# Kernel tuning notes

Measured on AMD Instinct MI355X. Metric: run time of the kernel, lower is better.

The kernel has to match this reference:

```python
import jax, jax.numpy as jnp
import numpy as np

B, T = 32, 64
INPUT_DIM, EMB, HA, HB, NUM_CLASS = 4894, 128, 128, 128, 1
D_IN = EMB + 1  # use_time=True appends scalar time feature


def gru_cell(x, h, Wih, Whh, bih, bhh):
    # torch nn.GRU cell semantics, gate order (r, z, n)
    gi = x @ Wih.T + bih
    gh = h @ Whh.T + bhh
    ir, iz, i_n = jnp.split(gi, 3, axis=-1)
    hr, hz, hn = jnp.split(gh, 3, axis=-1)
    r = jax.nn.sigmoid(ir + hr)
    z = jax.nn.sigmoid(iz + hz)
    n = jnp.tanh(i_n + r * hn)
    return (1.0 - z) * n + z * h


def setup_inputs():
    key = jax.random.key(0)
    ks = jax.random.split(key, 14)
    f32 = jnp.float32
    s = lambda k, sh, sc: (jax.random.normal(k, sh) * sc).astype(f32)
    return {
        "x": jax.random.uniform(ks[0], (B, T, INPUT_DIM), dtype=f32),
        "t": jax.random.uniform(ks[1], (B, T), dtype=f32),
        "lengths": jax.random.randint(ks[2], (B,), 1, T + 1),
        "W_emb": s(ks[3], (EMB, INPUT_DIM), 0.02),
        "Wih_a": s(ks[4], (3 * HA, D_IN), 0.05),
        "Whh_a": s(ks[5], (3 * HA, HA), 0.05),
        "bih_a": jnp.zeros((3 * HA,), f32),
        "bhh_a": jnp.zeros((3 * HA,), f32),
        "Wih_b": s(ks[6], (3 * HB, D_IN), 0.05),
        "Whh_b": s(ks[7], (3 * HB, HB), 0.05),
        "bih_b": jnp.zeros((3 * HB,), f32),
        "bhh_b": jnp.zeros((3 * HB,), f32),
        "w_alpha": s(ks[8], (1, HA), 0.1),
        "b_alpha": jnp.zeros((1,), f32),
        "W_beta": s(ks[9], (EMB, HB), 0.1),
        "b_beta": jnp.zeros((EMB,), f32),
        "W_out": s(ks[10], (NUM_CLASS, EMB), 0.1),
        "b_out": jnp.zeros((NUM_CLASS,), f32),
    }


def reference(x, t, lengths, W_emb, Wih_a, Whh_a, bih_a, bhh_a,
              Wih_b, Whh_b, bih_b, bhh_b, w_alpha, b_alpha,
              W_beta, b_beta, W_out, b_out):
    # embedding (dropout is identity in inference)
    emb = x @ W_emb.T                                   # [B,T,E]
    temb = jnp.concatenate([emb, t[..., None]], axis=-1)  # [B,T,E+1]

    # reversed-prefix tensor: R[b,i,k] = temb[b, i-k] for k<=i else 0
    i_idx = jnp.arange(T)[:, None]
    k_idx = jnp.arange(T)[None, :]
    src = i_idx - k_idx                                  # [T,T]
    valid = (src >= 0)
    src_c = jnp.clip(src, 0)
    vmask = valid[None, :, :, None].astype(emb.dtype)
    R = jnp.take(temb, src_c, axis=1) * vmask            # [B,T,T,D_IN]
    E_rev = jnp.take(emb, src_c, axis=1) * vmask         # [B,T,T,E]

    # run alpha/beta GRUs along the prefix axis k (causal, so zero padding
    # at k>i never affects the k<=i outputs that we keep)
    R_k = jnp.moveaxis(R, 2, 0)                          # [Tk,B,T,D_IN]
    h0a = jnp.zeros((B, T, HA), emb.dtype)
    h0b = jnp.zeros((B, T, HB), emb.dtype)

    def step(carry, xk):
        ha, hb = carry
        ha = gru_cell(xk, ha, Wih_a, Whh_a, bih_a, bhh_a)
        hb = gru_cell(xk, hb, Wih_b, Whh_b, bih_b, bhh_b)
        return (ha, hb), (ha, hb)

    _, (Ha, Hb) = jax.lax.scan(step, (h0a, h0b), R_k)
    Ha = jnp.moveaxis(Ha, 0, 2)                          # [B,T,Tk,HA]
    Hb = jnp.moveaxis(Hb, 0, 2)                          # [B,T,Tk,HB]

    # attention over the i+1 prefix positions
    scores = (Ha @ w_alpha.T + b_alpha)[..., 0]          # [B,T,Tk]
    scores = jnp.where(valid[None], scores, jnp.float32(-1e9))
    alpha = jax.nn.softmax(scores, axis=-1)
    beta = jnp.tanh(Hb @ W_beta.T + b_beta)              # [B,T,Tk,E]

    c = jnp.einsum('btk,btke,btke->bte', alpha, beta, E_rev)
    row_valid = (jnp.arange(T)[None, :] < lengths[:, None]).astype(c.dtype)
    c = c * row_valid[..., None]                         # zero where i >= lengths[b]

    logits = c @ W_out.T + b_out                         # [B,T,1]
    return logits[..., 0]
```

## Files before the change

kernel.cpp:

```cpp
#include <hip/hip_runtime.h>
#include <hip/hip_bf16.h>

#define DEVI __device__ __forceinline__

typedef __attribute__((ext_vector_type(8))) short short8;
typedef __attribute__((ext_vector_type(8))) unsigned short ushort8;
typedef __attribute__((ext_vector_type(4))) unsigned short ushort4v;
typedef __attribute__((ext_vector_type(2))) unsigned int u32x2;
typedef __attribute__((ext_vector_type(4))) float f32x4;

static constexpr int TT = 64, KIN = 4894, KINP = 4896, E = 128;
static constexpr float L2E = 1.4426950408889634f;

DEVI unsigned short f2bf(float f) {
    union { float f; unsigned u; } v; v.f = f;
    unsigned r = v.u + 0x7fffu + ((v.u >> 16) & 1u);
    return (unsigned short)(r >> 16);
}
DEVI float sigm2(float x) { return __builtin_amdgcn_rcpf(1.f + __builtin_amdgcn_exp2f(-x)); }
DEVI float tanh2(float x) { return 1.f - 2.f * __builtin_amdgcn_rcpf(__builtin_amdgcn_exp2f(x + x) + 1.f); }

DEVI void gload16(const float* g, float* l) {
    __builtin_amdgcn_global_load_lds(
        (const __attribute__((address_space(1))) void*)g,
        (__attribute__((address_space(3))) void*)l, 16, 0, 0);
}

DEVI short8 cvt8(const float* __restrict__ p, float s) {
    float2 v0 = *(const float2*)p, v1 = *(const float2*)(p + 2);
    float2 v2 = *(const float2*)(p + 4), v3 = *(const float2*)(p + 6);
    short8 r;
    r[0] = (short)f2bf(v0.x * s); r[1] = (short)f2bf(v0.y * s);
    r[2] = (short)f2bf(v1.x * s); r[3] = (short)f2bf(v1.y * s);
    r[4] = (short)f2bf(v2.x * s); r[5] = (short)f2bf(v2.y * s);
    r[6] = (short)f2bf(v3.x * s); r[7] = (short)f2bf(v3.y * s);
    return r;
}

__global__ void prep_kernel(const float* __restrict__ Wemb,
                            const float* __restrict__ Wih_a, const float* __restrict__ Wih_b,
                            const float* __restrict__ Whh_a, const float* __restrict__ Whh_b,
                            const float* __restrict__ Wbeta,
                            unsigned short* __restrict__ wembbf, unsigned short* __restrict__ wihbf,
                            unsigned short* __restrict__ whhbf, unsigned short* __restrict__ wbetabf) {
    int job = blockIdx.x * blockDim.x + threadIdx.x;
    const int JWE = 128 * 612, JWIH = 768 * 16, JWHH = 768 * 16, JWB = 128 * 16;
    if (job < JWE) {
        int row = job / 612, c8 = (job % 612) * 8;
        ushort8 v;
        #pragma unroll
        for (int jj = 0; jj < 8; ++jj) { int c = c8 + jj; v[jj] = (c < KIN) ? f2bf(Wemb[(long)row * KIN + c]) : (unsigned short)0; }
        *(ushort8*)(wembbf + (long)row * KINP + c8) = v;
        return;
    }
    job -= JWE;
    if (job < JWIH) {
        int g = job / 16, c8 = (job % 16) * 8;
        const float* src = (g < 384) ? (Wih_a + (long)g * 129) : (Wih_b + (long)(g - 384) * 129);
        ushort8 v;
        #pragma unroll
        for (int jj = 0; jj < 8; ++jj) v[jj] = f2bf(src[c8 + jj] * L2E);
        *(ushort8*)(wihbf + (long)g * 128 + c8) = v;
        return;
    }
    job -= JWIH;
    if (job < JWHH) {
        int g = job / 16, c8 = (job % 16) * 8;
        const float* src = (g < 384) ? (Whh_a + (long)g * 128) : (Whh_b + (long)(g - 384) * 128);
        ushort8 v;
        #pragma unroll
        for (int jj = 0; jj < 8; ++jj) v[jj] = f2bf(src[c8 + jj] * L2E);
        *(ushort8*)(whhbf + (long)g * 128 + c8) = v;
        return;
    }
    job -= JWHH;
    if (job < JWB) {
        int e = job / 16, c8 = (job % 16) * 8;
        ushort8 v;
        #pragma unroll
        for (int jj = 0; jj < 8; ++jj) v[jj] = f2bf(Wbeta[(long)e * 128 + c8 + jj] * L2E);
        *(ushort8*)(wbetabf + (long)e * 128 + c8) = v;
    }
}

__global__ __launch_bounds__(256) void emb_gemm(const float* __restrict__ x,
                                                const unsigned short* __restrict__ wembbf,
                                                float* __restrict__ pout) {
    const int ks = blockIdx.x & 3, m0 = (blockIdx.x >> 2) * 16;
    const int w = threadIdx.x >> 6, l = threadIdx.x & 63, lr = l & 15, lo = l >> 4;
    const int n0 = (2 * w) * 16 + lr, n1 = (2 * w + 1) * 16 + lr;
    const float* xrow = x + (long)(m0 + lr) * KIN;
    const int k0 = ks * 1216;
    f32x4 acc0 = {0, 0, 0, 0}, acc1 = {0, 0, 0, 0};
    #pragma unroll 2
    for (int kt = 0; kt < 38; ++kt) {
        int k = k0 + kt * 32 + lo * 8;
        short8 a = cvt8(xrow + k, 1.f);
        short8 b0 = *(const short8*)(wembbf + (long)n0 * KINP + k);
        short8 b1 = *(const short8*)(wembbf + (long)n1 * KINP + k);
        acc0 = __builtin_amdgcn_mfma_f32_16x16x32_bf16(a, b0, acc0, 0, 0, 0);
        acc1 = __builtin_amdgcn_mfma_f32_16x16x32_bf16(a, b1, acc1, 0, 0, 0);
    }
    if (ks == 3) {
        int k = 4864 + lo * 8;
        short8 a;
        #pragma unroll
        for (int jj = 0; jj < 8; ++jj) { int c = k + jj; a[jj] = (c < KIN) ? (short)f2bf(xrow[c]) : (short)0; }
        short8 b0 = *(const short8*)(wembbf + (long)n0 * KINP + k);
        short8 b1 = *(const short8*)(wembbf + (long)n1 * KINP + k);
        acc0 = __builtin_amdgcn_mfma_f32_16x16x32_bf16(a, b0, acc0, 0, 0, 0);
        acc1 = __builtin_amdgcn_mfma_f32_16x16x32_bf16(a, b1, acc1, 0, 0, 0);
    }
    float* pbase = pout + (long)ks * 2048 * E;
    #pragma unroll
    for (int r = 0; r < 4; ++r) {
        int m = m0 + lo * 4 + r;
        pbase[(long)m * E + n0] = acc0[r];
        pbase[(long)m * E + n1] = acc1[r];
    }
}

__global__ __launch_bounds__(256) void emb_reduce(const float* __restrict__ pout,
                                                  float* __restrict__ emb_swz, unsigned short* __restrict__ embbf) {
    const long idx = (long)blockIdx.x * 256 + threadIdx.x;
    const long base = idx * 4;
    f32x4 s = *(const f32x4*)(pout + base);
    #pragma unroll
    for (int ks = 1; ks < 4; ++ks) {
        f32x4 v = *(const f32x4*)(pout + (long)ks * 2048 * E + base);
        s[0] += v[0]; s[1] += v[1]; s[2] += v[2]; s[3] += v[3];
    }
    const long tok = base >> 7;
    const int e0 = (int)(base & 127);
    const int cc = (int)((tok >> 6) & 15);
    *(f32x4*)(emb_swz + (tok << 7) + (e0 ^ ((cc & 7) << 2))) = s;
    ushort4v h;
    #pragma unroll
    for (int jj = 0; jj < 4; ++jj) h[jj] = f2bf(s[jj]);
    *(ushort4v*)(embbf + base) = h;
}

__global__ __launch_bounds__(256) void gi_gemm(const unsigned short* __restrict__ embbf,
                                               const unsigned short* __restrict__ wihbf,
                                               const float* __restrict__ Wih_a, const float* __restrict__ Wih_b,
                                               const float* __restrict__ t,
                                               const float* __restrict__ bih_a, const float* __restrict__ bih_b,
                                               const float* __restrict__ bhh_a, const float* __restrict__ bhh_b,
                                               float* __restrict__ Gi3) {
    const int m0 = blockIdx.x * 16;
    const int w = threadIdx.x >> 6, l = threadIdx.x & 63, lr = l & 15, lo = l >> 4;
    f32x4 acc[12];
    #pragma unroll
    for (int nl = 0; nl < 12; ++nl) acc[nl] = (f32x4){0, 0, 0, 0};
    #pragma unroll
    for (int kt = 0; kt < 4; ++kt) {
        int k = kt * 32 + lo * 8;
        short8 a0 = *(const short8*)(embbf + (long)(m0 + lr) * E + k);
        #pragma unroll
        for (int nl = 0; nl < 12; ++nl) {
            int n = (w * 12 + nl) * 16 + lr;
            short8 bf = *(const short8*)(wihbf + (long)n * 128 + k);
            acc[nl] = __builtin_amdgcn_mfma_f32_16x16x32_bf16(a0, bf, acc[nl], 0, 0, 0);
        }
    }
    #pragma unroll
    for (int nl = 0; nl < 12; ++nl) {
        int n = (w * 12 + nl) * 16 + lr;
        int gru = (n >= 384) ? 1 : 0;
        int nn = n - gru * 384;
        int gt = nn >> 7, u = nn & 127;
        float bias = (gru ? bih_b[nn] : bih_a[nn]);
        if (gt < 2) bias += (gru ? bhh_b[nn] : bhh_a[nn]);
        float cw = (n < 384) ? Wih_a[(long)n * 129 + 128] : Wih_b[(long)(n - 384) * 129 + 128];
        #pragma unroll
        for (int r = 0; r < 4; ++r) {
            int tok = m0 + lo * 4 + r;
            int cc = (tok >> 6) & 15;
            Gi3[(((long)tok * 2 + gru) * 3 + gt) * 128 + (u ^ ((cc & 7) << 2))] =
                acc[nl][r] + (bias + t[tok] * cw) * L2E;
        }
    }
}

__global__ __launch_bounds__(512, 1)
void retain_rec(const unsigned short* __restrict__ whhbf, const unsigned short* __restrict__ wbetabf,
                const float* __restrict__ Gi3, const float* __restrict__ emb_swz,
                const float* __restrict__ bhh_a, const float* __restrict__ bhh_b,
                const float* __restrict__ w_alpha, const float* __restrict__ b_alpha,
                const float* __restrict__ b_beta, const float* __restrict__ Wout,
                float* __restrict__ p_g, float* __restrict__ d_g) {
    const int tid = threadIdx.x;
    const int w = tid >> 6, l = tid & 63, lr = l & 15, lo = l >> 4;
    const int i = blockIdx.x >> 2, q = (blockIdx.x >> 1) & 1, g = blockIdx.x & 1;
    const int u0 = w * 16 + lo * 4;
    const int sw2 = (lr & 7) << 2;
    const int cS = tid >> 5, chk = tid & 31;

    __shared__ __align__(16) float Gst[2][3][16][128];
    __shared__ __align__(16) float Est[2][16][128];
    __shared__ __align__(16) unsigned short Hbf[2][16][128];
    __shared__ __align__(16) unsigned short Mld[2][16][128];
    __shared__ float pd_s[16][66];

    for (int idx = tid; idx < 2 * 16 * 128; idx += 512) (&Hbf[0][0][0])[idx] = 0;

    short8 Wf[3][4];
    #pragma unroll
    for (int gt = 0; gt < 3; ++gt)
        #pragma unroll
        for (int kt = 0; kt < 4; ++kt)
            Wf[gt][kt] = *(const short8*)(whhbf + (long)(g * 384 + gt * 128 + w * 16 + lr) * 128 + kt * 32 + lo * 8);
    short8 Xf[4];
    #pragma unroll
    for (int kt = 0; kt < 4; ++kt)
        Xf[kt] = g ? *(const short8*)(wbetabf + (long)(w * 16 + lr) * 128 + kt * 32 + lo * 8)
                   : cvt8(w_alpha + kt * 32 + lo * 8, L2E);
    short8 ones;
    #pragma unroll
    for (int jj = 0; jj < 8; ++jj) ones[jj] = (short)0x3F80;

    const float* bhhG = g ? bhh_b : bhh_a;
    f32x4 bhn4 = *(const f32x4*)(bhhG + 256 + u0);
    #pragma unroll
    for (int r = 0; r < 4; ++r) bhn4[r] *= L2E;
    f32x4 bb4 = {0, 0, 0, 0}, wo4 = {0, 0, 0, 0};
    if (g) {
        bb4 = *(const f32x4*)(b_beta + u0);
        #pragma unroll
        for (int r = 0; r < 4; ++r) bb4[r] *= L2E;
        wo4 = *(const f32x4*)(Wout + u0);
    }
    const float balL = b_alpha[0] * L2E;

    float h_old[4] = {0, 0, 0, 0};

    const long chainBase = (long)((q * 16 + cS) * 64);
    auto STAGE = [&](int b, int jg, int je) {
        const float* gb = Gi3 + ((chainBase + jg) * 2 + g) * 384 + chk * 4;
        float* lds0 = (float*)&Gst[b][0][0][0] + (w << 8);
        gload16(gb, lds0);
        gload16(gb + 128, (float*)&Gst[b][1][0][0] + (w << 8));
        gload16(gb + 256, (float*)&Gst[b][2][0][0] + (w << 8));
        if (g) gload16(emb_swz + ((chainBase + je) << 7) + chk * 4, (float*)&Est[b][0][0] + (w << 8));
    };

    STAGE(0, i, (i + 1 > 63) ? 63 : i + 1);

    const int iend = i + 1 + g;
    for (int n = 0; n <= iend; ++n) {
        __syncthreads();

        {
            int jg = i - n - 1; if (jg < 0) jg = 0;
            int je = i - n;     if (je < 0) je = 0;
            STAGE((n + 1) & 1, jg, je);
        }

        const int rb = n & 1, wb = rb ^ 1, bufc = n & 1;
        const bool do_gate = (n <= i);
        const bool do_post = (n >= 1) && (n <= i + 1);

        if (g && w == 0 && n >= 2) {
            f32x4 dacc = {0, 0, 0, 0};
            #pragma unroll
            for (int kt = 0; kt < 4; ++kt) {
                int sw = (kt * 32 + lo * 8) ^ ((lr & 7) * 8);
                short8 bm = *(const short8*)(&Mld[wb][lr][sw]);
                dacc = __builtin_amdgcn_mfma_f32_16x16x32_bf16(ones, bm, dacc, 0, 0, 0);
            }
            if (lo == 0) pd_s[lr][n - 2] = dacc[0];
        }

        short8 Af[4];
        if (do_gate || do_post) {
            #pragma unroll
            for (int kt = 0; kt < 4; ++kt) {
                int sw = (kt * 32 + lo * 8) ^ ((lr & 7) * 8);
                Af[kt] = *(const short8*)(&Hbf[rb][lr][sw]);
            }
        }

        f32x4 gh0 = {0, 0, 0, 0}, gh1 = {0, 0, 0, 0}, gh2 = bhn4;
        if (do_gate) {
            f32x4 a0 = {0, 0, 0, 0}, a1 = {0, 0, 0, 0}, a2 = {0, 0, 0, 0};
            #pragma unroll
            for (int kt = 0; kt < 2; ++kt) {
                gh0 = __builtin_amdgcn_mfma_f32_16x16x32_bf16(Wf[0][kt], Af[kt], gh0, 0, 0, 0);
                gh1 = __builtin_amdgcn_mfma_f32_16x16x32_bf16(Wf[1][kt], Af[kt], gh1, 0, 0, 0);
                gh2 = __builtin_amdgcn_mfma_f32_16x16x32_bf16(Wf[2][kt], Af[kt], gh2, 0, 0, 0);
                a0 = __builtin_amdgcn_mfma_f32_16x16x32_bf16(Wf[0][kt + 2], Af[kt + 2], a0, 0, 0, 0);
                a1 = __builtin_amdgcn_mfma_f32_16x16x32_bf16(Wf[1][kt + 2], Af[kt + 2], a1, 0, 0, 0);
                a2 = __builtin_amdgcn_mfma_f32_16x16x32_bf16(Wf[2][kt + 2], Af[kt + 2], a2, 0, 0, 0);
            }
            #pragma unroll
            for (int r = 0; r < 4; ++r) { gh0[r] += a0[r]; gh1[r] += a1[r]; gh2[r] += a2[r]; }
        }

        if (do_post) {
            f32x4 xacc = {0, 0, 0, 0}, xb = {0, 0, 0, 0};
            #pragma unroll
            for (int kt = 0; kt < 2; ++kt) {
                xacc = __builtin_amdgcn_mfma_f32_16x16x32_bf16(Xf[kt], Af[kt], xacc, 0, 0, 0);
                xb   = __builtin_amdgcn_mfma_f32_16x16x32_bf16(Xf[kt + 2], Af[kt + 2], xb, 0, 0, 0);
            }
            #pragma unroll
            for (int r = 0; r < 4; ++r) xacc[r] += xb[r];
            if (!g) {
                if (w == 0 && lo == 0) pd_s[lr][n - 1] = __builtin_amdgcn_exp2f(xacc[0] + balL);
            } else {
                f32x4 ev4 = *(const f32x4*)(&Est[bufc][lr][u0 ^ sw2]);
                float m0v = tanh2(xacc[0] + bb4[0]) * ev4[0] * wo4[0];
                float m1v = tanh2(xacc[1] + bb4[1]) * ev4[1] * wo4[1];
                float m2v = tanh2(xacc[2] + bb4[2]) * ev4[2] * wo4[2];
                float m3v = tanh2(xacc[3] + bb4[3]) * ev4[3] * wo4[3];
                unsigned mp0, mp1;
                asm("v_cvt_pk_bf16_f32 %0, %1, %2" : "=v"(mp0) : "v"(m0v), "v"(m1v));
                asm("v_cvt_pk_bf16_f32 %0, %1, %2" : "=v"(mp1) : "v"(m2v), "v"(m3v));
                *(u32x2*)(&Mld[rb][lr][u0 ^ ((lr & 7) * 8)]) = (u32x2){mp0, mp1};
            }
        }

        if (do_gate) {
            f32x4 gr = *(const f32x4*)(&Gst[bufc][0][lr][u0 ^ sw2]);
            f32x4 gz = *(const f32x4*)(&Gst[bufc][1][lr][u0 ^ sw2]);
            f32x4 gn = *(const f32x4*)(&Gst[bufc][2][lr][u0 ^ sw2]);
            float hn[4];
            #pragma unroll
            for (int r = 0; r < 4; ++r) {
                float rr = sigm2(gr[r] + gh0[r]);
                float zz = sigm2(gz[r] + gh1[r]);
                float nv = tanh2(gn[r] + rr * gh2[r]);
                float h = nv + zz * (h_old[r] - nv);
                h_old[r] = h;
                hn[r] = h;
            }
            unsigned p0, p1;
            asm("v_cvt_pk_bf16_f32 %0, %1, %2" : "=v"(p0) : "v"(hn[0]), "v"(hn[1]));
            asm("v_cvt_pk_bf16_f32 %0, %1, %2" : "=v"(p1) : "v"(hn[2]), "v"(hn[3]));
            *(u32x2*)(&Hbf[wb][lr][u0 ^ ((lr & 7) * 8)]) = (u32x2){p0, p1};
        }
    }

    __syncthreads();

    float* dst = g ? d_g : p_g;
    for (int idx = tid; idx < 16 * 64; idx += 512) {
        int c = idx >> 6, kk = idx & 63;
        if (kk <= i) {
            long row = (long)(q * 16 + c) * 64 + i;
            dst[row * 64 + kk] = pd_s[c][kk];
        }
    }
}

__global__ __launch_bounds__(512) void reduce_out(const float* __restrict__ p_g, const float* __restrict__ d_g,
                                                  const int* __restrict__ lengths, const float* __restrict__ b_out,
                                                  float* __restrict__ out) {
    const int w = threadIdx.x >> 6, l = threadIdx.x & 63;
    const int row = blockIdx.x * 8 + w;
    const int b = row >> 6, i = row & 63;
    float p = (l <= i) ? p_g[(long)row * 64 + l] : 0.f;
    float d = (l <= i) ? d_g[(long)row * 64 + l] : 0.f;
    float pd = p * d;
    #pragma unroll
    for (int off = 1; off < 64; off <<= 1) {
        p += __shfl_xor(p, off);
        pd += __shfl_xor(pd, off);
    }
    if (l == 0) {
        float val = (i < lengths[b]) ? pd / p + b_out[0] : b_out[0];
        out[row] = val;
    }
}

extern "C" void kernel_launch(void* const* d_in, const int* in_sizes, int n_in,
                              void* d_out, int out_size, void* d_ws, size_t ws_size,
                              hipStream_t stream) {
    (void)in_sizes; (void)n_in; (void)out_size; (void)ws_size;
    const float* x       = (const float*)d_in[0];
    const float* t       = (const float*)d_in[1];
    const int*   len     = (const int*)d_in[2];
    const float* Wemb    = (const float*)d_in[3];
    const float* Wih_a   = (const float*)d_in[4];
    const float* Whh_a   = (const float*)d_in[5];
    const float* bih_a   = (const float*)d_in[6];
    const float* bhh_a   = (const float*)d_in[7];
    const float* Wih_b   = (const float*)d_in[8];
    const float* Whh_b   = (const float*)d_in[9];
    const float* bih_b   = (const float*)d_in[10];
    const float* bhh_b   = (const float*)d_in[11];
    const float* w_alpha = (const float*)d_in[12];
    const float* b_alpha = (const float*)d_in[13];
    const float* W_beta  = (const float*)d_in[14];
    const float* b_beta  = (const float*)d_in[15];
    const float* W_out   = (const float*)d_in[16];
    const float* b_out   = (const float*)d_in[17];

    char* ws = (char*)d_ws;
    float*          emb_swz = (float*)(ws + 0);
    unsigned short* embbf   = (unsigned short*)(ws + 1048576);
    float*          Gi3     = (float*)(ws + 1572864);
    unsigned short* wembbf  = (unsigned short*)(ws + 7864320);
    unsigned short* wihbf   = (unsigned short*)(ws + 9117696);
    unsigned short* whhbf   = (unsigned short*)(ws + 9314304);
    unsigned short* wbetabf = (unsigned short*)(ws + 9510912);
    float*          p_g     = (float*)(ws + 9543680);
    float*          d_g     = (float*)(ws + 10067968);
    float*          pout    = (float*)(ws + 10592256);

    const int jobs = 128 * 612 + 768 * 16 + 768 * 16 + 128 * 16;
    prep_kernel<<<(jobs + 255) / 256, 256, 0, stream>>>(Wemb, Wih_a, Wih_b, Whh_a, Whh_b, W_beta,
                                                        wembbf, wihbf, whhbf, wbetabf);
    emb_gemm<<<512, 256, 0, stream>>>(x, wembbf, pout);
    emb_reduce<<<256, 256, 0, stream>>>(pout, emb_swz, embbf);
    gi_gemm<<<128, 256, 0, stream>>>(embbf, wihbf, Wih_a, Wih_b, t, bih_a, bih_b, bhh_a, bhh_b, Gi3);
    retain_rec<<<256, 512, 0, stream>>>(whhbf, wbetabf, Gi3, emb_swz, bhh_a, bhh_b,
                                        w_alpha, b_alpha, b_beta, W_out, p_g, d_g);
    reduce_out<<<256, 512, 0, stream>>>(p_g, d_g, len, b_out, (float*)d_out);
}
```

Baseline: 134.6 us.

## Fuse emb reduce into gi_gemm, prefold W_out, triple-buffer recurrence staging

```diff
diff --git a/kernel.cpp b/kernel.cpp
--- a/kernel.cpp
+++ b/kernel.cpp
@@ -5,7 +5,6 @@
 
 typedef __attribute__((ext_vector_type(8))) short short8;
 typedef __attribute__((ext_vector_type(8))) unsigned short ushort8;
-typedef __attribute__((ext_vector_type(4))) unsigned short ushort4v;
 typedef __attribute__((ext_vector_type(2))) unsigned int u32x2;
 typedef __attribute__((ext_vector_type(4))) float f32x4;
 
@@ -35,6 +34,16 @@
     r[4] = (short)f2bf(v2.x * s); r[5] = (short)f2bf(v2.y * s);
     r[6] = (short)f2bf(v3.x * s); r[7] = (short)f2bf(v3.y * s);
     return r;
+}
+DEVI short8 cvt8pk(const float* __restrict__ p) {
+    float2 v0 = *(const float2*)p, v1 = *(const float2*)(p + 2);
+    float2 v2 = *(const float2*)(p + 4), v3 = *(const float2*)(p + 6);
+    union { unsigned u[4]; short8 s; } o;
+    asm("v_cvt_pk_bf16_f32 %0, %1, %2" : "=v"(o.u[0]) : "v"(v0.x), "v"(v0.y));
+    asm("v_cvt_pk_bf16_f32 %0, %1, %2" : "=v"(o.u[1]) : "v"(v1.x), "v"(v1.y));
+    asm("v_cvt_pk_bf16_f32 %0, %1, %2" : "=v"(o.u[2]) : "v"(v2.x), "v"(v2.y));
+    asm("v_cvt_pk_bf16_f32 %0, %1, %2" : "=v"(o.u[3]) : "v"(v3.x), "v"(v3.y));
+    return o.s;
 }
 
 __global__ void prep_kernel(const float* __restrict__ Wemb,
@@ -95,7 +104,7 @@
     #pragma unroll 2
     for (int kt = 0; kt < 38; ++kt) {
         int k = k0 + kt * 32 + lo * 8;
-        short8 a = cvt8(xrow + k, 1.f);
+        short8 a = cvt8pk(xrow + k);
         short8 b0 = *(const short8*)(wembbf + (long)n0 * KINP + k);
         short8 b1 = *(const short8*)(wembbf + (long)n1 * KINP + k);
         acc0 = __builtin_amdgcn_mfma_f32_16x16x32_bf16(a, b0, acc0, 0, 0, 0);
@@ -120,42 +129,54 @@
     }
 }
 
-__global__ __launch_bounds__(256) void emb_reduce(const float* __restrict__ pout,
-                                                  float* __restrict__ emb_swz, unsigned short* __restrict__ embbf) {
-    const long idx = (long)blockIdx.x * 256 + threadIdx.x;
-    const long base = idx * 4;
-    f32x4 s = *(const f32x4*)(pout + base);
-    #pragma unroll
-    for (int ks = 1; ks < 4; ++ks) {
-        f32x4 v = *(const f32x4*)(pout + (long)ks * 2048 * E + base);
-        s[0] += v[0]; s[1] += v[1]; s[2] += v[2]; s[3] += v[3];
-    }
-    const long tok = base >> 7;
-    const int e0 = (int)(base & 127);
-    const int cc = (int)((tok >> 6) & 15);
-    *(f32x4*)(emb_swz + (tok << 7) + (e0 ^ ((cc & 7) << 2))) = s;
-    ushort4v h;
-    #pragma unroll
-    for (int jj = 0; jj < 4; ++jj) h[jj] = f2bf(s[jj]);
-    *(ushort4v*)(embbf + base) = h;
-}
-
-__global__ __launch_bounds__(256) void gi_gemm(const unsigned short* __restrict__ embbf,
+__global__ __launch_bounds__(256) void gi_gemm(const float* __restrict__ pout,
                                                const unsigned short* __restrict__ wihbf,
                                                const float* __restrict__ Wih_a, const float* __restrict__ Wih_b,
                                                const float* __restrict__ t,
                                                const float* __restrict__ bih_a, const float* __restrict__ bih_b,
                                                const float* __restrict__ bhh_a, const float* __restrict__ bhh_b,
-                                               float* __restrict__ Gi3) {
+                                               const float* __restrict__ Wout,
+                                               float* __restrict__ emb_swz_wo, float* __restrict__ Gi3) {
     const int m0 = blockIdx.x * 16;
-    const int w = threadIdx.x >> 6, l = threadIdx.x & 63, lr = l & 15, lo = l >> 4;
+    const int tid = threadIdx.x;
+    const int w = tid >> 6, l = tid & 63, lr = l & 15, lo = l >> 4;
+    __shared__ __align__(16) unsigned short embs[16][128];
+
+    {
+        const int trow = tid >> 4, e0 = (tid & 15) * 8;
+        const int tok = m0 + trow;
+        const long base = (long)tok * E + e0;
+        f32x4 s0 = *(const f32x4*)(pout + base);
+        f32x4 s1 = *(const f32x4*)(pout + base + 4);
+        #pragma unroll
+        for (int ks = 1; ks < 4; ++ks) {
+            f32x4 v0 = *(const f32x4*)(pout + (long)ks * 2048 * E + base);
+            f32x4 v1 = *(const f32x4*)(pout + (long)ks * 2048 * E + base + 4);
+            #pragma unroll
+            for (int jj = 0; jj < 4; ++jj) { s0[jj] += v0[jj]; s1[jj] += v1[jj]; }
+        }
+        ushort8 h;
+        #pragma unroll
+        for (int jj = 0; jj < 4; ++jj) { h[jj] = f2bf(s0[jj]); h[4 + jj] = f2bf(s1[jj]); }
+        *(ushort8*)(&embs[trow][e0]) = h;
+        f32x4 wo0 = *(const f32x4*)(Wout + e0);
+        f32x4 wo1 = *(const f32x4*)(Wout + e0 + 4);
+        #pragma unroll
+        for (int jj = 0; jj < 4; ++jj) { s0[jj] *= wo0[jj]; s1[jj] *= wo1[jj]; }
+        const int cc = (tok >> 6) & 15;
+        const int x0 = e0 ^ ((cc & 7) << 2), x1 = (e0 + 4) ^ ((cc & 7) << 2);
+        *(f32x4*)(emb_swz_wo + (long)tok * E + x0) = s0;
+        *(f32x4*)(emb_swz_wo + (long)tok * E + x1) = s1;
+    }
+    __syncthreads();
+
     f32x4 acc[12];
     #pragma unroll
     for (int nl = 0; nl < 12; ++nl) acc[nl] = (f32x4){0, 0, 0, 0};
     #pragma unroll
     for (int kt = 0; kt < 4; ++kt) {
         int k = kt * 32 + lo * 8;
-        short8 a0 = *(const short8*)(embbf + (long)(m0 + lr) * E + k);
+        short8 a0 = *(const short8*)(&embs[lr][k]);
         #pragma unroll
         for (int nl = 0; nl < 12; ++nl) {
             int n = (w * 12 + nl) * 16 + lr;
@@ -184,10 +205,10 @@
 
 __global__ __launch_bounds__(512, 1)
 void retain_rec(const unsigned short* __restrict__ whhbf, const unsigned short* __restrict__ wbetabf,
-                const float* __restrict__ Gi3, const float* __restrict__ emb_swz,
+                const float* __restrict__ Gi3, const float* __restrict__ emb_swz_wo,
                 const float* __restrict__ bhh_a, const float* __restrict__ bhh_b,
                 const float* __restrict__ w_alpha, const float* __restrict__ b_alpha,
-                const float* __restrict__ b_beta, const float* __restrict__ Wout,
+                const float* __restrict__ b_beta,
                 float* __restrict__ p_g, float* __restrict__ d_g) {
     const int tid = threadIdx.x;
     const int w = tid >> 6, l = tid & 63, lr = l & 15, lo = l >> 4;
@@ -196,8 +217,8 @@
     const int sw2 = (lr & 7) << 2;
     const int cS = tid >> 5, chk = tid & 31;
 
-    __shared__ __align__(16) float Gst[2][3][16][128];
-    __shared__ __align__(16) float Est[2][16][128];
+    __shared__ __align__(16) float Gst[3][3][16][128];
+    __shared__ __align__(16) float Est[3][16][128];
     __shared__ __align__(16) unsigned short Hbf[2][16][128];
     __shared__ __align__(16) unsigned short Mld[2][16][128];
     __shared__ float pd_s[16][66];
@@ -223,12 +244,11 @@
     f32x4 bhn4 = *(const f32x4*)(bhhG + 256 + u0);
     #pragma unroll
     for (int r = 0; r < 4; ++r) bhn4[r] *= L2E;
-    f32x4 bb4 = {0, 0, 0, 0}, wo4 = {0, 0, 0, 0};
+    f32x4 bb4 = {0, 0, 0, 0};
     if (g) {
         bb4 = *(const f32x4*)(b_beta + u0);
         #pragma unroll
         for (int r = 0; r < 4; ++r) bb4[r] *= L2E;
-        wo4 = *(const f32x4*)(Wout + u0);
     }
     const float balL = b_alpha[0] * L2E;
 
@@ -237,28 +257,31 @@
     const long chainBase = (long)((q * 16 + cS) * 64);
     auto STAGE = [&](int b, int jg, int je) {
         const float* gb = Gi3 + ((chainBase + jg) * 2 + g) * 384 + chk * 4;
-        float* lds0 = (float*)&Gst[b][0][0][0] + (w << 8);
-        gload16(gb, lds0);
-        gload16(gb + 128, (float*)&Gst[b][1][0][0] + (w << 8));
-        gload16(gb + 256, (float*)&Gst[b][2][0][0] + (w << 8));
-        if (g) gload16(emb_swz + ((chainBase + je) << 7) + chk * 4, (float*)&Est[b][0][0] + (w << 8));
+        gload16(gb,        (float*)&Gst[b][0][0][0] + (w << 8));
+        gload16(gb + 128,  (float*)&Gst[b][1][0][0] + (w << 8));
+        gload16(gb + 256,  (float*)&Gst[b][2][0][0] + (w << 8));
+        if (g) gload16(emb_swz_wo + ((chainBase + je) << 7) + chk * 4, (float*)&Est[b][0][0] + (w << 8));
     };
 
     STAGE(0, i, (i + 1 > 63) ? 63 : i + 1);
+    STAGE(1, (i - 1 < 0) ? 0 : i - 1, i);
+    if (g) asm volatile("s_waitcnt lgkmcnt(0) vmcnt(4)" ::: "memory");
+    else   asm volatile("s_waitcnt lgkmcnt(0) vmcnt(3)" ::: "memory");
+    __builtin_amdgcn_s_barrier();
+    __builtin_amdgcn_sched_barrier(0);
 
     const int iend = i + 1 + g;
     for (int n = 0; n <= iend; ++n) {
-        __syncthreads();
-
-        {
-            int jg = i - n - 1; if (jg < 0) jg = 0;
-            int je = i - n;     if (je < 0) je = 0;
-            STAGE((n + 1) & 1, jg, je);
-        }
-
-        const int rb = n & 1, wb = rb ^ 1, bufc = n & 1;
+        const int bufc = n % 3, bufs = (n + 2) % 3;
+        const int rb = n & 1, wb = rb ^ 1;
         const bool do_gate = (n <= i);
         const bool do_post = (n >= 1) && (n <= i + 1);
+
+        {
+            int jg = i - n - 2; if (jg < 0) jg = 0;
+            int je = i - n - 1; if (je < 0) je = 0;
+            STAGE(bufs, jg, je);
+        }
 
         if (g && w == 0 && n >= 2) {
             f32x4 dacc = {0, 0, 0, 0};
@@ -308,11 +331,11 @@
             if (!g) {
                 if (w == 0 && lo == 0) pd_s[lr][n - 1] = __builtin_amdgcn_exp2f(xacc[0] + balL);
             } else {
-                f32x4 ev4 = *(const f32x4*)(&Est[bufc][lr][u0 ^ sw2]);
-                float m0v = tanh2(xacc[0] + bb4[0]) * ev4[0] * wo4[0];
-                float m1v = tanh2(xacc[1] + bb4[1]) * ev4[1] * wo4[1];
-                float m2v = tanh2(xacc[2] + bb4[2]) * ev4[2] * wo4[2];
-                float m3v = tanh2(xacc[3] + bb4[3]) * ev4[3] * wo4[3];
+                f32x4 ew4 = *(const f32x4*)(&Est[bufc][lr][u0 ^ sw2]);
+                float m0v = tanh2(xacc[0] + bb4[0]) * ew4[0];
+                float m1v = tanh2(xacc[1] + bb4[1]) * ew4[1];
+                float m2v = tanh2(xacc[2] + bb4[2]) * ew4[2];
+                float m3v = tanh2(xacc[3] + bb4[3]) * ew4[3];
                 unsigned mp0, mp1;
                 asm("v_cvt_pk_bf16_f32 %0, %1, %2" : "=v"(mp0) : "v"(m0v), "v"(m1v));
                 asm("v_cvt_pk_bf16_f32 %0, %1, %2" : "=v"(mp1) : "v"(m2v), "v"(m3v));
@@ -339,6 +362,11 @@
             asm("v_cvt_pk_bf16_f32 %0, %1, %2" : "=v"(p1) : "v"(hn[2]), "v"(hn[3]));
             *(u32x2*)(&Hbf[wb][lr][u0 ^ ((lr & 7) * 8)]) = (u32x2){p0, p1};
         }
+
+        if (g) asm volatile("s_waitcnt lgkmcnt(0) vmcnt(4)" ::: "memory");
+        else   asm volatile("s_waitcnt lgkmcnt(0) vmcnt(3)" ::: "memory");
+        __builtin_amdgcn_s_barrier();
+        __builtin_amdgcn_sched_barrier(0);
     }
 
     __syncthreads();
@@ -398,23 +426,22 @@
 
     char* ws = (char*)d_ws;
     float*          emb_swz = (float*)(ws + 0);
-    unsigned short* embbf   = (unsigned short*)(ws + 1048576);
-    float*          Gi3     = (float*)(ws + 1572864);
-    unsigned short* wembbf  = (unsigned short*)(ws + 7864320);
-    unsigned short* wihbf   = (unsigned short*)(ws + 9117696);
-    unsigned short* whhbf   = (unsigned short*)(ws + 9314304);
-    unsigned short* wbetabf = (unsigned short*)(ws + 9510912);
-    float*          p_g     = (float*)(ws + 9543680);
-    float*          d_g     = (float*)(ws + 10067968);
-    float*          pout    = (float*)(ws + 10592256);
+    float*          Gi3     = (float*)(ws + 1048576);
+    unsigned short* wembbf  = (unsigned short*)(ws + 7340032);
+    unsigned short* wihbf   = (unsigned short*)(ws + 8593408);
+    unsigned short* whhbf   = (unsigned short*)(ws + 8790016);
+    unsigned short* wbetabf = (unsigned short*)(ws + 8986624);
+    float*          p_g     = (float*)(ws + 9019392);
+    float*          d_g     = (float*)(ws + 9543680);
+    float*          pout    = (float*)(ws + 10067968);
 
     const int jobs = 128 * 612 + 768 * 16 + 768 * 16 + 128 * 16;
     prep_kernel<<<(jobs + 255) / 256, 256, 0, stream>>>(Wemb, Wih_a, Wih_b, Whh_a, Whh_b, W_beta,
                                                         wembbf, wihbf, whhbf, wbetabf);
     emb_gemm<<<512, 256, 0, stream>>>(x, wembbf, pout);
-    emb_reduce<<<256, 256, 0, stream>>>(pout, emb_swz, embbf);
-    gi_gemm<<<128, 256, 0, stream>>>(embbf, wihbf, Wih_a, Wih_b, t, bih_a, bih_b, bhh_a, bhh_b, Gi3);
+    gi_gemm<<<128, 256, 0, stream>>>(pout, wihbf, Wih_a, Wih_b, t, bih_a, bih_b, bhh_a, bhh_b,
+                                     W_out, emb_swz, Gi3);
     retain_rec<<<256, 512, 0, stream>>>(whhbf, wbetabf, Gi3, emb_swz, bhh_a, bhh_b,
-                                        w_alpha, b_alpha, b_beta, W_out, p_g, d_g);
+                                        w_alpha, b_alpha, b_beta, p_g, d_g);
     reduce_out<<<256, 512, 0, stream>>>(p_g, d_g, len, b_out, (float*)d_out);
 }
```

After: 134.4 us. No clear change (-0.1%).
